# Kernel optimization log

Hardware: AMD Instinct MI355X
Metric: run time of the kernel (lower is better)

## Reference

```python
import jax, jax.numpy as jnp
import numpy as np

K = 3  # kernel size
PAD = 1
C_IN = 32
C_OUT = 32
CKK = C_IN * K * K  # 288
HID = C_OUT  # hidden width of kernel-generator MLP


def _unfold(x):
    """torch F.unfold equivalent, (C, kh, kw)-major. x: [B,C,H,W] -> [B, C*K*K, H*W]."""
    B, C, H, W = x.shape
    xp = jnp.pad(x, ((0, 0), (0, 0), (PAD, PAD), (PAD, PAD)))
    # stack K*K shifted views -> [B, C, K*K, H, W]
    patches = jnp.stack(
        [xp[:, :, i:i + H, j:j + W] for i in range(K) for j in range(K)], axis=2
    )
    return patches.reshape(B, C * K * K, H * W)


def setup_inputs() -> dict:
    key = jax.random.key(0)
    ks = jax.random.split(key, 6)
    B, H, W = 2, 64, 64
    x = jax.random.normal(ks[0], (B, C_IN, H, W), dtype=jnp.float32)
    # kernel_generator: Linear(CKK -> HID), Tanh, Linear(HID -> C_OUT*CKK)
    s1 = 1.0 / np.sqrt(CKK)
    s2 = 1.0 / np.sqrt(HID)
    W1 = jax.random.uniform(ks[1], (HID, CKK), jnp.float32, -s1, s1)
    b1 = jax.random.uniform(ks[2], (HID,), jnp.float32, -s1, s1)
    W2 = jax.random.uniform(ks[3], (C_OUT * CKK, HID), jnp.float32, -s2, s2)
    b2 = jax.random.uniform(ks[4], (C_OUT * CKK,), jnp.float32, -s2, s2)
    bias = jax.random.uniform(ks[5], (C_OUT,), jnp.float32, -s1, s1)
    return {"x": x, "W1": W1, "b1": b1, "W2": W2, "b2": b2, "bias": bias}


def reference(x, W1, b1, W2, b2, bias):
    B, C, H, W = x.shape
    L = H * W
    u = _unfold(x)                       # [B, CKK, L]
    ut = u.transpose(0, 2, 1)            # [B, L, CKK]
    h = jnp.tanh(jnp.einsum('blj,hj->blh', ut, W1) + b1)          # [B, L, HID]
    kern = jnp.einsum('blh,oh->blo', h, W2) + b2                  # [B, L, C_OUT*CKK]
    kern = kern.reshape(B, L, C_OUT, CKK)                         # per-pixel kernels
    out = jnp.einsum('bloj,blj->bol', kern, ut)                   # [B, C_OUT, L]
    out = out.reshape(B, C_OUT, H, W) + bias[None, :, None, None]
    return out
```

## Files before the change

kernel.cpp:

```cpp
#include <hip/hip_runtime.h>
#include <hip/hip_bf16.h>


#define CKK 288
#define SJ  296

typedef __attribute__((ext_vector_type(8))) short short8;
typedef __attribute__((ext_vector_type(4))) float f32x4;

#define W2F_OFF 0
#define W1B_OFF 294912
#define B2B_OFF (294912 + 9216)

__device__ __forceinline__ short f2bf(float f) {
    __hip_bfloat16 h = __float2bfloat16(f);
    return __builtin_bit_cast(short, h);
}

__global__ __launch_bounds__(256) void prep_kernel(
    const float* __restrict__ W1, const float* __restrict__ W2,
    const float* __restrict__ b2, __hip_bfloat16* __restrict__ ws)
{
    const int t = threadIdx.x;
    if (blockIdx.x < 32) {
        __shared__ float lds_f[32 * 289];
        const int o = blockIdx.x;
        #pragma unroll
        for (int k = 0; k < 36; ++k) {
            int idx = k * 256 + t;
            int j = idx >> 5, h = idx & 31;
            lds_f[h * 289 + j] = W2[o * 9216 + idx];
        }
        __syncthreads();
        #pragma unroll
        for (int k = 0; k < 5; ++k) {
            int c = k * 256 + t;
            if (c < 1152) {
                int nf = c / 576, rem = c - nf * 576;
                int kb = rem >> 6, l = rem & 63;
                int h  = nf * 16 + (l & 15);
                int j0 = kb * 32 + ((l >> 4) << 3);
                short8 v;
                #pragma unroll
                for (int e = 0; e < 8; ++e)
                    v[e] = f2bf(lds_f[h * 289 + j0 + e]);
                *(short8*)(ws + W2F_OFF + (size_t)(o * 9216) + c * 8) = v;
            }
        }
    } else if (blockIdx.x < 40) {
        int b0 = (blockIdx.x - 32) * 1152;
        #pragma unroll
        for (int k = 0; k < 5; ++k) {
            int c = k * 256 + t;
            if (c < 1152) ws[W1B_OFF + b0 + c] = __float2bfloat16(W1[b0 + c]);
        }
    } else if (blockIdx.x < 48) {
        int b0 = (blockIdx.x - 40) * 1152;
        #pragma unroll
        for (int k = 0; k < 5; ++k) {
            int c = k * 256 + t;
            if (c < 1152) ws[B2B_OFF + b0 + c] = __float2bfloat16(b2[b0 + c]);
        }
    }
}

__global__ __launch_bounds__(256, 4) void dynaconv_main(
    const float* __restrict__ x,
    const float* __restrict__ b1,
    const float* __restrict__ bias,
    const __hip_bfloat16* __restrict__ ws,
    float* __restrict__ out)
{
    __shared__ __hip_bfloat16 u_lds[32 * SJ];
    __shared__ float hh_lds[32 * 33];
    __shared__ float t_lds[32 * 8];
    __shared__ float o_stage[8][32];

    const int t  = threadIdx.x;
    const int w  = t >> 6;
    const int l  = t & 63;
    const int lg = l >> 4;
    const int lr = l & 15;

    const int nt = blockIdx.x & 3, mt = blockIdx.x >> 2;
    const int o0 = nt * 8;
    const int g0 = mt * 32;
    const int b  = g0 >> 12;
    const int l0 = g0 & 4095;
    const int y  = l0 >> 6;
    const int wx0 = l0 & 63;

    #pragma unroll
    for (int k = 0; k < 36; ++k) {
        int idx = k * 256 + t;
        int j = idx >> 5, p = idx & 31;
        int c = j / 9, r = j - c * 9;
        int ki = r / 3, kj = r - ki * 3;
        int y2 = y + ki - 1;
        int x2 = wx0 + p + kj - 1;
        float v = 0.f;
        if ((unsigned)y2 < 64u && (unsigned)x2 < 64u)
            v = x[((b * 32 + c) * 64 + y2) * 64 + x2];
        u_lds[p * SJ + j] = __float2bfloat16(v);
    }
    __syncthreads();

    if (w < 3) {
        const __hip_bfloat16* w1b = ws + W1B_OFF;
        const __hip_bfloat16* b2b = ws + B2B_OFF;
        f32x4 acc0 = {0.f,0.f,0.f,0.f}, acc1 = {0.f,0.f,0.f,0.f};
        #pragma unroll
        for (int kb = 0; kb < 9; ++kb) {
            short8 bf;
            if (w < 2)
                bf = *(const short8*)(w1b + (w * 16 + lr) * CKK + kb * 32 + lg * 8);
            else if (lr < 8)
                bf = *(const short8*)(b2b + (o0 + lr) * CKK + kb * 32 + lg * 8);
            else
                bf = short8{0,0,0,0,0,0,0,0};
            short8 a0 = *(const short8*)(u_lds + lr * SJ + kb * 32 + lg * 8);
            short8 a1 = *(const short8*)(u_lds + (16 + lr) * SJ + kb * 32 + lg * 8);
            acc0 = __builtin_amdgcn_mfma_f32_16x16x32_bf16(a0, bf, acc0, 0, 0, 0);
            acc1 = __builtin_amdgcn_mfma_f32_16x16x32_bf16(a1, bf, acc1, 0, 0, 0);
        }
        if (w < 2) {
            const int col = w * 16 + lr;
            float b1v = b1[col];
            #pragma unroll
            for (int r = 0; r < 4; ++r) {
                hh_lds[(lg * 4 + r) * 33 + col]      = tanhf(acc0[r] + b1v);
                hh_lds[(16 + lg * 4 + r) * 33 + col] = tanhf(acc1[r] + b1v);
            }
        } else if (lr < 8) {
            float bv = bias[o0 + lr];
            #pragma unroll
            for (int r = 0; r < 4; ++r) {
                t_lds[(lg * 4 + r) * 8 + lr]      = acc0[r] + bv;
                t_lds[(16 + lg * 4 + r) * 8 + lr] = acc1[r] + bv;
            }
        }
    }
    __syncthreads();

    f32x4 acc[2][4];
    #pragma unroll
    for (int m = 0; m < 2; ++m)
        #pragma unroll
        for (int nf = 0; nf < 4; ++nf)
            acc[m][nf] = f32x4{0.f, 0.f, 0.f, 0.f};

    {
        const __hip_bfloat16* W2f = ws + W2F_OFF;
        const int ckbase = (o0 * 2 + w * 4) * 9;
        short8 bcur[4];
        #pragma unroll
        for (int nf = 0; nf < 4; ++nf)
            bcur[nf] = *(const short8*)(W2f + (size_t)(ckbase + nf * 9) * 512 + l * 8);

        #pragma unroll
        for (int kb = 0; kb < 9; ++kb) {
            short8 a0 = *(const short8*)(u_lds + lr * SJ + kb * 32 + lg * 8);
            short8 a1 = *(const short8*)(u_lds + (16 + lr) * SJ + kb * 32 + lg * 8);
            short8 bnext[4];
            if (kb < 8) {
                #pragma unroll
                for (int nf = 0; nf < 4; ++nf)
                    bnext[nf] = *(const short8*)(W2f + (size_t)(ckbase + nf * 9 + kb + 1) * 512 + l * 8);
            }
            #pragma unroll
            for (int nf = 0; nf < 4; ++nf) {
                acc[0][nf] = __builtin_amdgcn_mfma_f32_16x16x32_bf16(a0, bcur[nf], acc[0][nf], 0, 0, 0);
                acc[1][nf] = __builtin_amdgcn_mfma_f32_16x16x32_bf16(a1, bcur[nf], acc[1][nf], 0, 0, 0);
            }
            if (kb < 8) {
                #pragma unroll
                for (int nf = 0; nf < 4; ++nf)
                    bcur[nf] = bnext[nf];
            }
        }
    }

    #pragma unroll
    for (int ol = 0; ol < 2; ++ol) {
        const int o_loc = w * 2 + ol;
        #pragma unroll
        for (int m = 0; m < 2; ++m) {
            #pragma unroll
            for (int r = 0; r < 4; ++r) {
                const int p = m * 16 + lg * 4 + r;
                float v = hh_lds[p * 33 + lr]      * acc[m][ol * 2][r]
                        + hh_lds[p * 33 + 16 + lr] * acc[m][ol * 2 + 1][r];
                v += __shfl_xor(v, 1);
                v += __shfl_xor(v, 2);
                v += __shfl_xor(v, 4);
                v += __shfl_xor(v, 8);
                if (lr == 0) o_stage[o_loc][p] = v;
            }
        }
    }
    __syncthreads();

    {
        int o_l = t >> 5, p = t & 31;
        float val = o_stage[o_l][p] + t_lds[p * 8 + o_l];
        out[((size_t)(b * 32 + o0 + o_l)) * 4096 + l0 + p] = val;
    }
}

extern "C" void kernel_launch(void* const* d_in, const int* in_sizes, int n_in,
                              void* d_out, int out_size, void* d_ws, size_t ws_size,
                              hipStream_t stream) {
    const float* x    = (const float*)d_in[0];
    const float* W1   = (const float*)d_in[1];
    const float* b1   = (const float*)d_in[2];
    const float* W2   = (const float*)d_in[3];
    const float* b2   = (const float*)d_in[4];
    const float* bias = (const float*)d_in[5];
    float* out = (float*)d_out;
    __hip_bfloat16* ws = (__hip_bfloat16*)d_ws;

    prep_kernel<<<48, 256, 0, stream>>>(W1, W2, b2, ws);
    dynaconv_main<<<1024, 256, 0, stream>>>(x, b1, bias, ws, out);
}
```

Before: 31.15 us.

## Fuse weight-prep into main kernel with global atomic flag handoff

Merges the separate weight-conversion kernel into the main dynamic-conv kernel. The first 48 blocks convert W1, W2 and b2 to bf16 in the workspace and then bump a global atomic counter. Every block stages its unfold tile and spins on that counter before its GEMMs. This removes one kernel launch boundary and overlaps prep with the input loads, but adds a memset, spin-waits, and a dependence on the prep blocks being resident early (a possible deadlock risk if scheduling order is not guaranteed).

```diff
diff --git a/kernel.cpp b/kernel.cpp
--- a/kernel.cpp
+++ b/kernel.cpp
@@ -11,72 +11,81 @@
 #define W2F_OFF 0
 #define W1B_OFF 294912
 #define B2B_OFF (294912 + 9216)
+#define FLAG_BYTE 626688
+
+#define SMEM_BYTES 36992
+#define U_B   0
+#define HH_B  18944
+#define T_B   23168
+#define O_B   24192
 
 __device__ __forceinline__ short f2bf(float f) {
     __hip_bfloat16 h = __float2bfloat16(f);
     return __builtin_bit_cast(short, h);
 }
 
-__global__ __launch_bounds__(256) void prep_kernel(
-    const float* __restrict__ W1, const float* __restrict__ W2,
-    const float* __restrict__ b2, __hip_bfloat16* __restrict__ ws)
+__global__ __launch_bounds__(256, 4) void dynaconv_fused(
+    const float* __restrict__ x,    const float* __restrict__ W1,
+    const float* __restrict__ b1,   const float* __restrict__ W2,
+    const float* __restrict__ b2,   const float* __restrict__ bias,
+    __hip_bfloat16* __restrict__ ws, float* __restrict__ out)
 {
+    __shared__ __align__(16) char smem[SMEM_BYTES];
     const int t = threadIdx.x;
-    if (blockIdx.x < 32) {
-        __shared__ float lds_f[32 * 289];
-        const int o = blockIdx.x;
-        #pragma unroll
-        for (int k = 0; k < 36; ++k) {
-            int idx = k * 256 + t;
-            int j = idx >> 5, h = idx & 31;
-            lds_f[h * 289 + j] = W2[o * 9216 + idx];
+    unsigned int* flag = (unsigned int*)((char*)ws + FLAG_BYTE);
+
+    if (blockIdx.x < 48) {
+        if (blockIdx.x < 32) {
+            float* lds_f = (float*)smem;
+            const int o = blockIdx.x;
+            #pragma unroll
+            for (int k = 0; k < 36; ++k) {
+                int idx = k * 256 + t;
+                int j = idx >> 5, h = idx & 31;
+                lds_f[h * 289 + j] = W2[o * 9216 + idx];
+            }
+            __syncthreads();
+            #pragma unroll
+            for (int k = 0; k < 5; ++k) {
+                int c = k * 256 + t;
+                if (c < 1152) {
+                    int nf = c / 576, rem = c - nf * 576;
+                    int kb = rem >> 6, l = rem & 63;
+                    int h  = nf * 16 + (l & 15);
+                    int j0 = kb * 32 + ((l >> 4) << 3);
+                    short8 v;
+                    #pragma unroll
+                    for (int e = 0; e < 8; ++e)
+                        v[e] = f2bf(lds_f[h * 289 + j0 + e]);
+                    *(short8*)(ws + W2F_OFF + (size_t)(o * 9216) + c * 8) = v;
+                }
+            }
+        } else if (blockIdx.x < 40) {
+            int b0 = (blockIdx.x - 32) * 1152;
+            #pragma unroll
+            for (int k = 0; k < 5; ++k) {
+                int c = k * 256 + t;
+                if (c < 1152) ws[W1B_OFF + b0 + c] = __float2bfloat16(W1[b0 + c]);
+            }
+        } else {
+            int b0 = (blockIdx.x - 40) * 1152;
+            #pragma unroll
+            for (int k = 0; k < 5; ++k) {
+                int c = k * 256 + t;
+                if (c < 1152) ws[B2B_OFF + b0 + c] = __float2bfloat16(b2[b0 + c]);
+            }
         }
         __syncthreads();
-        #pragma unroll
-        for (int k = 0; k < 5; ++k) {
-            int c = k * 256 + t;
-            if (c < 1152) {
-                int nf = c / 576, rem = c - nf * 576;
-                int kb = rem >> 6, l = rem & 63;
-                int h  = nf * 16 + (l & 15);
-                int j0 = kb * 32 + ((l >> 4) << 3);
-                short8 v;
-                #pragma unroll
-                for (int e = 0; e < 8; ++e)
-                    v[e] = f2bf(lds_f[h * 289 + j0 + e]);
-                *(short8*)(ws + W2F_OFF + (size_t)(o * 9216) + c * 8) = v;
-            }
-        }
-    } else if (blockIdx.x < 40) {
-        int b0 = (blockIdx.x - 32) * 1152;
-        #pragma unroll
-        for (int k = 0; k < 5; ++k) {
-            int c = k * 256 + t;
-            if (c < 1152) ws[W1B_OFF + b0 + c] = __float2bfloat16(W1[b0 + c]);
-        }
-    } else if (blockIdx.x < 48) {
-        int b0 = (blockIdx.x - 40) * 1152;
-        #pragma unroll
-        for (int k = 0; k < 5; ++k) {
-            int c = k * 256 + t;
-            if (c < 1152) ws[B2B_OFF + b0 + c] = __float2bfloat16(b2[b0 + c]);
-        }
-    }
-}
-
-__global__ __launch_bounds__(256, 4) void dynaconv_main(
-    const float* __restrict__ x,
-    const float* __restrict__ b1,
-    const float* __restrict__ bias,
-    const __hip_bfloat16* __restrict__ ws,
-    float* __restrict__ out)
-{
-    __shared__ __hip_bfloat16 u_lds[32 * SJ];
-    __shared__ float hh_lds[32 * 33];
-    __shared__ float t_lds[32 * 8];
-    __shared__ float o_stage[8][32];
-
-    const int t  = threadIdx.x;
+        if (t == 0)
+            __hip_atomic_fetch_add(flag, 1u, __ATOMIC_RELEASE,
+                                   __HIP_MEMORY_SCOPE_AGENT);
+    }
+
+    __hip_bfloat16* u_lds = (__hip_bfloat16*)(smem + U_B);
+    float* hh_lds  = (float*)(smem + HH_B);
+    float* t_lds   = (float*)(smem + T_B);
+    float* o_stage = (float*)(smem + O_B);
+
     const int w  = t >> 6;
     const int l  = t & 63;
     const int lg = l >> 4;
@@ -103,6 +112,12 @@
             v = x[((b * 32 + c) * 64 + y2) * 64 + x2];
         u_lds[p * SJ + j] = __float2bfloat16(v);
     }
+
+    if (t == 0) {
+        while (__hip_atomic_load(flag, __ATOMIC_ACQUIRE,
+                                 __HIP_MEMORY_SCOPE_AGENT) < 48u)
+            __builtin_amdgcn_s_sleep(8);
+    }
     __syncthreads();
 
     if (w < 3) {
@@ -194,7 +209,7 @@
                 v += __shfl_xor(v, 2);
                 v += __shfl_xor(v, 4);
                 v += __shfl_xor(v, 8);
-                if (lr == 0) o_stage[o_loc][p] = v;
+                if (lr == 0) o_stage[o_loc * 32 + p] = v;
             }
         }
     }
@@ -202,7 +217,7 @@
 
     {
         int o_l = t >> 5, p = t & 31;
-        float val = o_stage[o_l][p] + t_lds[p * 8 + o_l];
+        float val = o_stage[o_l * 32 + p] + t_lds[p * 8 + o_l];
         out[((size_t)(b * 32 + o0 + o_l)) * 4096 + l0 + p] = val;
     }
 }
@@ -219,6 +234,6 @@
     float* out = (float*)d_out;
     __hip_bfloat16* ws = (__hip_bfloat16*)d_ws;
 
-    prep_kernel<<<48, 256, 0, stream>>>(W1, W2, b2, ws);
-    dynaconv_main<<<1024, 256, 0, stream>>>(x, b1, bias, ws, out);
+    hipMemsetAsync((char*)d_ws + FLAG_BYTE, 0, 4, stream);
+    dynaconv_fused<<<1024, 256, 0, stream>>>(x, W1, b1, W2, b2, bias, ws, out);
 }
```

New measurement: 35.37 us. +13.5%, slower.
